# Kernel optimization log

Measured on AMD Instinct MI355X. Metric: run time of the kernel, lower is better.

The kernel has to match this reference:

```python
import jax, jax.numpy as jnp
import numpy as np

N = 10000          # num_nodes
E_DIR = 160000     # directed random edges before symmetrization
B = 8              # batch
IN = 64            # input_size per node
UNITS = 64         # num_units
K = 2              # max_diffusion_step -> num_matrices = K + 1
LAMBDA_MAX = 1.5   # stand-in for eigsh largest-eigenvalue estimate


def _build_scaled_laplacian():
    # L_scaled = (2/lambda_max) * (I - D^-1/2 A D^-1/2) - I, as sparse COO
    rng = np.random.default_rng(0)
    src = rng.integers(0, N, E_DIR)
    dst = rng.integers(0, N, E_DIR)
    # symmetrize A = max(A, A^T) by duplicating edges both ways
    r = np.concatenate([src, dst])
    c = np.concatenate([dst, src])
    w = np.ones(2 * E_DIR, np.float32)
    deg = np.zeros(N, np.float32)
    np.add.at(deg, r, w)
    d_inv_sqrt = np.where(deg > 0, deg ** -0.5, 0.0).astype(np.float32)
    coef = np.float32(2.0 / LAMBDA_MAX)
    off_vals = (-coef * d_inv_sqrt[r] * d_inv_sqrt[c] * w).astype(np.float32)
    diag_idx = np.arange(N, dtype=np.int32)
    diag_vals = np.full(N, coef - 1.0, np.float32)
    rows = np.concatenate([r.astype(np.int32), diag_idx])
    cols = np.concatenate([c.astype(np.int32), diag_idx])
    vals = np.concatenate([off_vals, diag_vals])
    return rows, cols, vals  # nnz = 2*E_DIR + N = 330000


def setup_inputs() -> dict:
    key = jax.random.key(0)
    k_in, k_w = jax.random.split(key)
    rows, cols, vals = _build_scaled_laplacian()
    num_matrices = K + 1
    fan_in = IN * num_matrices
    xavier = np.sqrt(6.0 / (fan_in + UNITS)).astype(np.float32)
    return {
        "inputs": jax.random.normal(k_in, (B, N * IN), dtype=jnp.float32),
        "rows": jnp.asarray(rows),
        "cols": jnp.asarray(cols),
        "vals": jnp.asarray(vals),
        "weights": jax.random.uniform(k_w, (fan_in, UNITS), dtype=jnp.float32,
                                      minval=-xavier, maxval=xavier),
        "biases": jnp.zeros((UNITS,), dtype=jnp.float32),
    }


def reference(inputs, rows, cols, vals, weights, biases):
    batch = inputs.shape[0]
    x = inputs.reshape(batch, N, -1)              # [B, N, in]
    in_size = x.shape[2]
    # x0: [N, in*B]
    x0 = jnp.transpose(x, (1, 2, 0)).reshape(N, in_size * batch)

    def spmm(h):  # sparse Laplacian @ dense
        return jax.ops.segment_sum(vals[:, None] * h[cols], rows, num_segments=N)

    # Chebyshev recursion: T0 = x0, T1 = L x0, Tk = 2 L Tk-1 - Tk-2
    xs = [x0]
    x1 = spmm(x0)
    xs.append(x1)
    xk_1, xk_2 = x1, x0
    for _ in range(2, K + 1):
        x2 = 2.0 * spmm(xk_1) - xk_2
        xs.append(x2)
        xk_1, xk_2 = x2, xk_1

    num_matrices = K + 1
    xcat = jnp.stack(xs, axis=0)                              # [M, N, in*B]
    xcat = xcat.reshape(num_matrices, N, in_size, batch)      # [M, N, in, B]
    xcat = jnp.transpose(xcat, (3, 1, 2, 0))                  # [B, N, in, M]
    xcat = xcat.reshape(batch * N, in_size * num_matrices)
    out = xcat @ weights + biases
    return out.reshape(batch, N, UNITS)
```

## Files before the change

### kernel.cpp

```cpp
#include <hip/hip_runtime.h>
#include <hip/hip_fp16.h>

#define N_NODES 10000
#define BATCH   8
#define IN_SZ   64
#define UNITS   64
#define ROW_U   256
#define RCAP    96
#define STR     (N_NODES * 64)

typedef unsigned int uint;
typedef unsigned short ushort;
typedef __attribute__((ext_vector_type(8))) _Float16 half8;
typedef __attribute__((ext_vector_type(4))) float float4v;
typedef __attribute__((ext_vector_type(2))) float float2v;

__device__ inline uint f2bf_bits(float f) {
    uint u = __float_as_uint(f);
    uint r = ((u >> 16) & 1u) + 0x7FFFu;
    return (u + r) >> 16;
}
__device__ inline uint pack2h(float a, float b) {
    return (uint)__half_as_ushort(__float2half(a)) |
           ((uint)__half_as_ushort(__float2half(b)) << 16);
}
__device__ inline float h_lo(uint u) {
    return __half2float(__ushort_as_half((ushort)(u & 0xFFFFu)));
}
__device__ inline float h_hi(uint u) {
    return __half2float(__ushort_as_half((ushort)(u >> 16)));
}

__global__ __launch_bounds__(256) void k_transpose_scatter(
    const float2v* __restrict__ in2, uint* __restrict__ x0,
    const int* __restrict__ rows, const int* __restrict__ cols,
    const float* __restrict__ vals, int* __restrict__ cursor,
    uint* __restrict__ edges, int nnz) {
    int gid = blockIdx.x * 256 + threadIdx.x;
    if (gid < nnz) {
        int r   = rows[gid];
        int pos = r * RCAP + atomicAdd(&cursor[r], 1);
        edges[pos] = (uint)cols[gid] | (f2bf_bits(vals[gid]) << 16);
    }
    int n  = gid >> 8;
    int b  = (gid >> 5) & 7;
    int iu = gid & 31;
    float2v v = __builtin_nontemporal_load(&in2[(size_t)b * (N_NODES * 32) +
                                                (size_t)n * 32 + iu]);
    int q = (gid >> 6) & 3;
    x0[(size_t)q * STR + (size_t)n * 64 + (gid & 63)] = pack2h(v.x, v.y);
}

__global__ __launch_bounds__(256) void k_spmm(const int* __restrict__ cursor,
                                              const uint* __restrict__ edges,
                                              const uint* __restrict__ xin,
                                              uint* __restrict__ xout,
                                              const uint* __restrict__ xsub,
                                              float scale) {
    int L    = blockIdx.x;
    int q    = (L & 7) >> 1;
    int rb   = ((L >> 3) << 1) | (L & 1);
    int wave = threadIdx.x >> 6;
    uint lane = threadIdx.x & 63;
    int row  = rb * 4 + wave;

    const uint* xq = xin + (size_t)q * STR;
    int base = row * RCAP;
    int cnt  = __builtin_amdgcn_readfirstlane(cursor[row]);

    float a0 = 0.f, a1 = 0.f;

    int full_end = base + (cnt & ~7);
    int e = base;
    for (; e < full_end; e += 8) {
        uint ep[8];
#pragma unroll
        for (int j = 0; j < 8; ++j) ep[j] = edges[e + j];
        uint x[8];
#pragma unroll
        for (int j = 0; j < 8; ++j)
            x[j] = xq[(ep[j] & 0x3FFFu) * 64u + lane];
#pragma unroll
        for (int j = 0; j < 8; ++j) {
            float vj = __uint_as_float(ep[j] & 0xFFFF0000u);
            a0 += vj * h_lo(x[j]);
            a1 += vj * h_hi(x[j]);
        }
    }
    int rem = cnt & 7;
    if (rem) {
        uint ep[8];
#pragma unroll
        for (int j = 0; j < 8; ++j) ep[j] = edges[e + j];
        uint x[8];
#pragma unroll
        for (int j = 0; j < 8; ++j) {
            uint c = ep[j] & 0x3FFFu;
            if (c > N_NODES - 1) c = N_NODES - 1;
            x[j] = xq[c * 64u + lane];
        }
#pragma unroll
        for (int j = 0; j < 8; ++j) {
            float vj = (j < rem) ? __uint_as_float(ep[j] & 0xFFFF0000u) : 0.f;
            a0 += vj * h_lo(x[j]);
            a1 += vj * h_hi(x[j]);
        }
    }

    float o0 = scale * a0, o1 = scale * a1;
    if (xsub) {
        uint sx = __builtin_nontemporal_load(
            &xsub[(size_t)q * STR + (size_t)row * 64 + lane]);
        o0 -= h_lo(sx);
        o1 -= h_hi(sx);
    }
    __builtin_nontemporal_store(pack2h(o0, o1),
        &xout[(size_t)q * STR + (size_t)row * 64 + lane]);
}

__global__ __launch_bounds__(256) void k_combine(const uint* __restrict__ x0,
                                                 const uint* __restrict__ x1,
                                                 const uint* __restrict__ x2,
                                                 const float* __restrict__ W,
                                                 const float* __restrict__ bias,
                                                 float* __restrict__ out) {
    __shared__ ushort sWt[64][200];
    int t = threadIdx.x;
    for (int e = t; e < 192 * 64; e += 256) {
        int f = e >> 6;
        int u = e & 63;
        int i = f / 3;
        int m = f - 3 * i;
        sWt[u][m * 64 + i] = __half_as_ushort(__float2half(W[e]));
    }
    __syncthreads();

    int wave = t >> 6, lane = t & 63;
    int mrow = lane & 15, quad = lane >> 4;
    int L    = blockIdx.x;
    int b    = L & 7;
    int n0   = (L >> 3) * 64 + wave * 16;

    const uint* xs[3] = {x0, x1, x2};
    int an = n0 + mrow;
    if (an > N_NODES - 1) an = N_NODES - 1;

    half8 af[6];
#pragma unroll
    for (int kb = 0; kb < 6; ++kb) {
        int mat = kb >> 1;
        int c_u = b * 32 + (kb & 1) * 16 + quad * 4;
        int q   = c_u >> 6;
        af[kb] = __builtin_nontemporal_load(
            (const half8*)(xs[mat] + (size_t)q * STR + (size_t)an * 64 +
                           (c_u & 63)));
    }

    float4v acc[4];
#pragma unroll
    for (int ut = 0; ut < 4; ++ut) acc[ut] = (float4v){0.f, 0.f, 0.f, 0.f};

#pragma unroll
    for (int kb = 0; kb < 6; ++kb)
#pragma unroll
        for (int ut = 0; ut < 4; ++ut)
            acc[ut] = __builtin_amdgcn_mfma_f32_16x16x32_f16(
                af[kb],
                *(const half8*)&sWt[ut * 16 + mrow][kb * 32 + quad * 8],
                acc[ut], 0, 0, 0);

#pragma unroll
    for (int ut = 0; ut < 4; ++ut) {
        float bv = bias[ut * 16 + mrow];
        int u = ut * 16 + mrow;
#pragma unroll
        for (int r = 0; r < 4; ++r) {
            int n = n0 + quad * 4 + r;
            if (n < N_NODES)
                __builtin_nontemporal_store(acc[ut][r] + bv,
                    &out[((size_t)b * N_NODES + n) * UNITS + u]);
        }
    }
}

extern "C" void kernel_launch(void* const* d_in, const int* in_sizes, int n_in,
                              void* d_out, int out_size, void* d_ws, size_t ws_size,
                              hipStream_t stream) {
    const float* inputs = (const float*)d_in[0];
    const int*   rows   = (const int*)d_in[1];
    const int*   cols   = (const int*)d_in[2];
    const float* vals   = (const float*)d_in[3];
    const float* W      = (const float*)d_in[4];
    const float* bias   = (const float*)d_in[5];
    float*       out    = (float*)d_out;
    int nnz = in_sizes[1];

    char* p = (char*)d_ws;
    auto alloc = [&](size_t bytes) {
        char* r = p;
        p += (bytes + 255) & ~(size_t)255;
        return r;
    };
    uint* x0     = (uint*)alloc(sizeof(uint) * (size_t)N_NODES * ROW_U);
    uint* x1     = (uint*)alloc(sizeof(uint) * (size_t)N_NODES * ROW_U);
    uint* x2     = (uint*)alloc(sizeof(uint) * (size_t)N_NODES * ROW_U);
    int*  cursor = (int*)alloc(sizeof(int) * N_NODES);
    uint* edges  = (uint*)alloc(sizeof(uint) * (size_t)N_NODES * RCAP);

    (void)hipMemsetAsync(cursor, 0, sizeof(int) * N_NODES, stream);
    k_transpose_scatter<<<N_NODES, 256, 0, stream>>>((const float2v*)inputs, x0,
                                                     rows, cols, vals, cursor,
                                                     edges, nnz);
    k_spmm<<<N_NODES, 256, 0, stream>>>(cursor, edges, x0, x1, nullptr, 1.0f);
    k_spmm<<<N_NODES, 256, 0, stream>>>(cursor, edges, x1, x2, x0, 2.0f);
    k_combine<<<157 * 8, 256, 0, stream>>>(x0, x1, x2, W, bias, out);
}
```

Before: 181.4 us.

## Double-buffer SpMM gathers, vectorize input transpose, overlap weight staging in combine

The SpMM loop now software-pipelines edge blocks with two register buffers, so the gather for the next block of 8 edges is issued before the FMAs for the current block. The tail is folded in through a per-edge mask, and the xsub load is hoisted to the start of the kernel. The transpose kernel reads float4 and writes packed 8-byte fp16 pairs with half as many blocks. The combine kernel issues its activation loads before staging W into shared memory so the two overlap. The cost is higher register pressure in the SpMM, which may lower occupancy.

```diff
diff --git a/kernel.cpp b/kernel.cpp
--- a/kernel.cpp
+++ b/kernel.cpp
@@ -13,7 +13,7 @@
 typedef unsigned short ushort;
 typedef __attribute__((ext_vector_type(8))) _Float16 half8;
 typedef __attribute__((ext_vector_type(4))) float float4v;
-typedef __attribute__((ext_vector_type(2))) float float2v;
+typedef __attribute__((ext_vector_type(2))) uint uint2v;
 
 __device__ inline uint f2bf_bits(float f) {
     uint u = __float_as_uint(f);
@@ -32,7 +32,7 @@
 }
 
 __global__ __launch_bounds__(256) void k_transpose_scatter(
-    const float2v* __restrict__ in2, uint* __restrict__ x0,
+    const float4v* __restrict__ in4, uint* __restrict__ x0,
     const int* __restrict__ rows, const int* __restrict__ cols,
     const float* __restrict__ vals, int* __restrict__ cursor,
     uint* __restrict__ edges, int nnz) {
@@ -42,14 +42,37 @@
         int pos = r * RCAP + atomicAdd(&cursor[r], 1);
         edges[pos] = (uint)cols[gid] | (f2bf_bits(vals[gid]) << 16);
     }
-    int n  = gid >> 8;
-    int b  = (gid >> 5) & 7;
-    int iu = gid & 31;
-    float2v v = __builtin_nontemporal_load(&in2[(size_t)b * (N_NODES * 32) +
-                                                (size_t)n * 32 + iu]);
-    int q = (gid >> 6) & 3;
-    x0[(size_t)q * STR + (size_t)n * 64 + (gid & 63)] = pack2h(v.x, v.y);
-}
+    int i4 = gid & 15;
+    int b  = (gid >> 4) & 7;
+    int n  = gid >> 7;
+    float4v v = __builtin_nontemporal_load(
+        &in4[((size_t)b * N_NODES + n) * 16 + i4]);
+    int c_u = b * 32 + i4 * 2;
+    int q   = c_u >> 6;
+    uint2v pk;
+    pk.x = pack2h(v.x, v.y);
+    pk.y = pack2h(v.z, v.w);
+    __builtin_nontemporal_store(pk,
+        (uint2v*)(x0 + (size_t)q * STR + (size_t)n * 64 + (c_u & 63)));
+}
+
+#define LOADE(EP, OFF)                                                        \
+    _Pragma("unroll") for (int j = 0; j < 8; ++j) EP[j] = edges[(OFF) + j];
+
+#define GATHERX(XR, EP)                                                       \
+    _Pragma("unroll") for (int j = 0; j < 8; ++j) {                           \
+        uint c = EP[j] & 0x3FFFu;                                             \
+        if (c > N_NODES - 1) c = N_NODES - 1;     \
+        XR[j] = xq[c * 64u + lane];              \
+    }
+
+#define FMA8(EP, XR, G0)                                                      \
+    _Pragma("unroll") for (int j = 0; j < 8; ++j) {                           \
+        uint vb = ((G0) + j < cnt) ? (EP[j] & 0xFFFF0000u) : 0u;    \
+        float vj = __uint_as_float(vb);                                       \
+        a0 += vj * h_lo(XR[j]);                            \
+        a1 += vj * h_hi(XR[j]);                            \
+    }
 
 __global__ __launch_bounds__(256) void k_spmm(const int* __restrict__ cursor,
                                               const uint* __restrict__ edges,
@@ -67,50 +90,35 @@
     const uint* xq = xin + (size_t)q * STR;
     int base = row * RCAP;
     int cnt  = __builtin_amdgcn_readfirstlane(cursor[row]);
+    int nblk = (cnt + 7) >> 3;
+
+    uint sx = 0;
+    if (xsub) sx = __builtin_nontemporal_load(
+        &xsub[(size_t)q * STR + (size_t)row * 64 + lane]);
 
     float a0 = 0.f, a1 = 0.f;
 
-    int full_end = base + (cnt & ~7);
-    int e = base;
-    for (; e < full_end; e += 8) {
-        uint ep[8];
-#pragma unroll
-        for (int j = 0; j < 8; ++j) ep[j] = edges[e + j];
-        uint x[8];
-#pragma unroll
-        for (int j = 0; j < 8; ++j)
-            x[j] = xq[(ep[j] & 0x3FFFu) * 64u + lane];
-#pragma unroll
-        for (int j = 0; j < 8; ++j) {
-            float vj = __uint_as_float(ep[j] & 0xFFFF0000u);
-            a0 += vj * h_lo(x[j]);
-            a1 += vj * h_hi(x[j]);
+    uint epA[8], epB[8];
+    uint xA[8], xB[8];
+
+    LOADE(epA, base);
+    GATHERX(xA, epA);
+
+    int k = 0;
+    for (; k + 2 <= nblk; k += 2) {
+        LOADE(epB, base + 8 * (k + 1));
+        GATHERX(xB, epB);
+        FMA8(epA, xA, 8 * k);
+        if (k + 2 < nblk) {
+            LOADE(epA, base + 8 * (k + 2));
+            GATHERX(xA, epA);
         }
-    }
-    int rem = cnt & 7;
-    if (rem) {
-        uint ep[8];
-#pragma unroll
-        for (int j = 0; j < 8; ++j) ep[j] = edges[e + j];
-        uint x[8];
-#pragma unroll
-        for (int j = 0; j < 8; ++j) {
-            uint c = ep[j] & 0x3FFFu;
-            if (c > N_NODES - 1) c = N_NODES - 1;
-            x[j] = xq[c * 64u + lane];
-        }
-#pragma unroll
-        for (int j = 0; j < 8; ++j) {
-            float vj = (j < rem) ? __uint_as_float(ep[j] & 0xFFFF0000u) : 0.f;
-            a0 += vj * h_lo(x[j]);
-            a1 += vj * h_hi(x[j]);
-        }
-    }
+        FMA8(epB, xB, 8 * (k + 1));
+    }
+    if (k < nblk) FMA8(epA, xA, 8 * k);
 
     float o0 = scale * a0, o1 = scale * a1;
     if (xsub) {
-        uint sx = __builtin_nontemporal_load(
-            &xsub[(size_t)q * STR + (size_t)row * 64 + lane]);
         o0 -= h_lo(sx);
         o1 -= h_hi(sx);
     }
@@ -125,16 +133,7 @@
                                                  const float* __restrict__ bias,
                                                  float* __restrict__ out) {
     __shared__ ushort sWt[64][200];
-    int t = threadIdx.x;
-    for (int e = t; e < 192 * 64; e += 256) {
-        int f = e >> 6;
-        int u = e & 63;
-        int i = f / 3;
-        int m = f - 3 * i;
-        sWt[u][m * 64 + i] = __half_as_ushort(__float2half(W[e]));
-    }
-    __syncthreads();
-
+    int t    = threadIdx.x;
     int wave = t >> 6, lane = t & 63;
     int mrow = lane & 15, quad = lane >> 4;
     int L    = blockIdx.x;
@@ -155,6 +154,15 @@
             (const half8*)(xs[mat] + (size_t)q * STR + (size_t)an * 64 +
                            (c_u & 63)));
     }
+
+    for (int e = t; e < 192 * 64; e += 256) {
+        int f = e >> 6;
+        int u = e & 63;
+        int i = f / 3;
+        int m = f - 3 * i;
+        sWt[u][m * 64 + i] = __half_as_ushort(__float2half(W[e]));
+    }
+    __syncthreads();
 
     float4v acc[4];
 #pragma unroll
@@ -208,9 +216,8 @@
     uint* edges  = (uint*)alloc(sizeof(uint) * (size_t)N_NODES * RCAP);
 
     (void)hipMemsetAsync(cursor, 0, sizeof(int) * N_NODES, stream);
-    k_transpose_scatter<<<N_NODES, 256, 0, stream>>>((const float2v*)inputs, x0,
-                                                     rows, cols, vals, cursor,
-                                                     edges, nnz);
+    k_transpose_scatter<<<N_NODES / 2, 256, 0, stream>>>(
+        (const float4v*)inputs, x0, rows, cols, vals, cursor, edges, nnz);
     k_spmm<<<N_NODES, 256, 0, stream>>>(cursor, edges, x0, x1, nullptr, 1.0f);
     k_spmm<<<N_NODES, 256, 0, stream>>>(cursor, edges, x1, x2, x0, 2.0f);
     k_combine<<<157 * 8, 256, 0, stream>>>(x0, x1, x2, W, bias, out);
```

Result: no change. 184.6 us (+1.8%).
